# Performance work log

Measured on AMD Instinct MI355X. Metric: run time of the kernel, lower is better.

Reference implementation:

```python
import jax, jax.numpy as jnp
import numpy as np

B, S, D, H, F = 8, 1024, 1024, 16, 4096
DH = D // H  # 64
EPS = 1e-12


def _layer_norm(x, g, b):
    mu = jnp.mean(x, axis=-1, keepdims=True)
    var = jnp.mean(jnp.square(x - mu), axis=-1, keepdims=True)
    return (x - mu) / jnp.sqrt(var + EPS) * g + b


def setup_inputs() -> dict:
    key = jax.random.key(0)
    ks = jax.random.split(key, 16)
    sd = 0.02
    inp = {
        "x": jax.random.normal(ks[0], (B, S, D), dtype=jnp.float32),
        "attn_mask": jnp.ones((B, S), dtype=jnp.int32),
        # attention projections (torch Linear: W is [out, in])
        "Wq": jax.random.normal(ks[1], (D, D), dtype=jnp.float32) * sd,
        "bq": jnp.zeros((D,), dtype=jnp.float32),
        "Wk": jax.random.normal(ks[2], (D, D), dtype=jnp.float32) * sd,
        "bk": jnp.zeros((D,), dtype=jnp.float32),
        "Wv": jax.random.normal(ks[3], (D, D), dtype=jnp.float32) * sd,
        "bv": jnp.zeros((D,), dtype=jnp.float32),
        "Wo": jax.random.normal(ks[4], (D, D), dtype=jnp.float32) * sd,
        "bo": jnp.zeros((D,), dtype=jnp.float32),
        # sa_layer_norm
        "ln1_g": jnp.ones((D,), dtype=jnp.float32),
        "ln1_b": jnp.zeros((D,), dtype=jnp.float32),
        # FFN
        "W1": jax.random.normal(ks[5], (F, D), dtype=jnp.float32) * sd,
        "b1": jnp.zeros((F,), dtype=jnp.float32),
        "W2": jax.random.normal(ks[6], (D, F), dtype=jnp.float32) * sd,
        "b2": jnp.zeros((D,), dtype=jnp.float32),
        # output_layer_norm
        "ln2_g": jnp.ones((D,), dtype=jnp.float32),
        "ln2_b": jnp.zeros((D,), dtype=jnp.float32),
    }
    return inp


def reference(x, attn_mask, Wq, bq, Wk, bk, Wv, bv, Wo, bo,
              ln1_g, ln1_b, W1, b1, W2, b2, ln2_g, ln2_b):
    b, s, d = x.shape

    def proj_heads(inp, W, bias):
        y = jnp.einsum('bsd,ed->bse', inp, W) + bias  # torch Linear: x @ W.T + b
        return y.reshape(b, s, H, DH).transpose(0, 2, 1, 3)  # (b, h, s, dh)

    q = proj_heads(x, Wq, bq) / jnp.sqrt(jnp.float32(DH))
    k = proj_heads(x, Wk, bk)
    v = proj_heads(x, Wv, bv)

    scores = jnp.einsum('bhqe,bhke->bhqk', q, k)  # (b, h, s, s)
    pad = (attn_mask == 0)[:, None, None, :]      # (b, 1, 1, s)
    scores = jnp.where(pad, -jnp.inf, scores)
    weights = jax.nn.softmax(scores, axis=-1)

    ctx = jnp.einsum('bhqk,bhke->bhqe', weights, v)
    ctx = ctx.transpose(0, 2, 1, 3).reshape(b, s, d)
    sa_out = jnp.einsum('bsd,ed->bse', ctx, Wo) + bo

    h = _layer_norm(sa_out + x, ln1_g, ln1_b)

    ff = jnp.einsum('bsd,fd->bsf', h, W1) + b1
    ff = jax.nn.gelu(ff, approximate=False)
    ff = jnp.einsum('bsf,df->bsd', ff, W2) + b2

    out = _layer_norm(ff + h, ln2_g, ln2_b)
    return out
```

## Files before the change

### kernel.cpp

```cpp
#include <hip/hip_runtime.h>
#include <math.h>

typedef __attribute__((ext_vector_type(8))) short short8;
typedef __attribute__((ext_vector_type(4))) float f32x4;

__device__ __forceinline__ unsigned short f2bf(float f) {
  unsigned int u = __float_as_uint(f);
  u += 0x7fffu + ((u >> 16) & 1u);
  return (unsigned short)(u >> 16);
}

__device__ __forceinline__ float gelu_f(float v) {
  float xa = fabsf(v) * 0.70710678118f;
  float t = __builtin_amdgcn_rcpf(1.f + 0.3275911f * xa);
  float p = t * (0.254829592f +
            t * (-0.284496736f +
            t * (1.421413741f +
            t * (-1.453152027f + t * 1.061405429f))));
  float erfa = 1.f - p * __expf(-xa * xa);
  return 0.5f * v * (1.f + copysignf(erfa, v));
}

__device__ __forceinline__ void gll16(const unsigned short* g, unsigned short* l) {
  __builtin_amdgcn_global_load_lds(
      (const __attribute__((address_space(1))) unsigned int*)(uintptr_t)g,
      (__attribute__((address_space(3))) unsigned int*)(uintptr_t)l, 16, 0, 0);
}

__global__ __launch_bounds__(256) void cvt_all(
    const float* __restrict__ Wq, const float* __restrict__ Wk,
    const float* __restrict__ Wv, const float* __restrict__ Wo,
    const float* __restrict__ W1, const float* __restrict__ W2,
    const float* __restrict__ x, unsigned short* __restrict__ ws) {
  const int bi = blockIdx.x;
  const float* in;
  unsigned short* out;
  int i;
  if (bi < 4096) {
    const int m = bi >> 10;
    in = (m == 0) ? Wq : (m == 1) ? Wk : (m == 2) ? Wv : Wo;
    out = ws + (size_t)m * (1u << 20);
    i = (bi & 1023) * 256 + threadIdx.x;
  } else if (bi < 8192) {
    in = W1; out = ws + (4u << 20); i = (bi - 4096) * 256 + threadIdx.x;
  } else if (bi < 12288) {
    in = W2; out = ws + (8u << 20); i = (bi - 8192) * 256 + threadIdx.x;
  } else {
    in = x; out = ws + (12u << 20); i = (bi - 12288) * 256 + threadIdx.x;
  }
  float4 f = reinterpret_cast<const float4*>(in)[i];
  ushort4 o;
  o.x = f2bf(f.x); o.y = f2bf(f.y); o.z = f2bf(f.z); o.w = f2bf(f.w);
  reinterpret_cast<ushort4*>(out)[i] = o;
}

template <int EPI, bool SWAP>
__global__ __launch_bounds__(256) void gemm_nt(
    const unsigned short* __restrict__ A, const unsigned short* __restrict__ B,
    const float* __restrict__ bias, const float* __restrict__ bias_k,
    int K, int N, const float* __restrict__ resid,
    unsigned short* __restrict__ outb, float* __restrict__ outf) {
  __shared__ __align__(16) unsigned short As[2][128 * 32];
  __shared__ __align__(16) unsigned short Bs[2][128 * 32];
  const int t = threadIdx.x;
  const int tm = blockIdx.y * 128, tn = blockIdx.x * 128;
  const int lane = t & 63, wv = t >> 6;
  const int wr = wv >> 1, wc = wv & 1;
  const int l15 = lane & 15, quad = lane >> 4;
  const int srow = lane >> 2;
  const int scol = (lane & 3) << 3;

  const unsigned short* pa0 = &A[(size_t)(tm + wv * 32 + srow) * K + scol];
  const unsigned short* pa1 = &A[(size_t)(tm + wv * 32 + 16 + srow) * K + scol];
  const unsigned short* pb0 = &B[(size_t)(tn + wv * 32 + srow) * K + scol];
  const unsigned short* pb1 = &B[(size_t)(tn + wv * 32 + 16 + srow) * K + scol];
  unsigned short* la0 = &As[0][(wv * 2) * 512];
  unsigned short* la1 = &As[0][(wv * 2 + 1) * 512];
  unsigned short* lb0 = &Bs[0][(wv * 2) * 512];
  unsigned short* lb1 = &Bs[0][(wv * 2 + 1) * 512];

  const f32x4 zero = {0.f, 0.f, 0.f, 0.f};
  f32x4 acc[4][4];
#pragma unroll
  for (int i = 0; i < 4; ++i)
#pragma unroll
    for (int j = 0; j < 4; ++j) acc[i][j] = zero;

  gll16(pa0, la0); pa0 += 32;
  gll16(pa1, la1); pa1 += 32;
  gll16(pb0, lb0); pb0 += 32;
  gll16(pb1, lb1); pb1 += 32;

  const int nIter = K >> 5;
  for (int it = 0; it < nIter; ++it) {
    __syncthreads();
    const int cur = (it & 1) * 4096;
    const int nxt = 4096 - cur;
    if (it + 1 < nIter) {
      gll16(pa0, la0 + nxt); pa0 += 32;
      gll16(pa1, la1 + nxt); pa1 += 32;
      gll16(pb0, lb0 + nxt); pb0 += 32;
      gll16(pb1, lb1 + nxt); pb1 += 32;
    }
    short8 af[4], bfr[4];
#pragma unroll
    for (int i = 0; i < 4; ++i) {
      af[i] = *reinterpret_cast<const short8*>(&As[0][cur + (wr * 64 + i * 16 + l15) * 32 + quad * 8]);
      bfr[i] = *reinterpret_cast<const short8*>(&Bs[0][cur + (wc * 64 + i * 16 + l15) * 32 + quad * 8]);
    }
#pragma unroll
    for (int i = 0; i < 4; ++i)
#pragma unroll
      for (int j = 0; j < 4; ++j)
        acc[i][j] = SWAP
            ? __builtin_amdgcn_mfma_f32_16x16x32_bf16(bfr[j], af[i], acc[i][j], 0, 0, 0)
            : __builtin_amdgcn_mfma_f32_16x16x32_bf16(af[i], bfr[j], acc[i][j], 0, 0, 0);
  }

  if (SWAP) {
#pragma unroll
    for (int i = 0; i < 4; ++i) {
      const int row = tm + wr * 64 + i * 16 + l15;
#pragma unroll
      for (int j = 0; j < 4; ++j) {
        const int col0 = tn + wc * 64 + j * 16 + quad * 4;
        if (EPI == 5) {
          const int chunk = col0 >> 10;
          const int colc = col0 & 1023;
          const float4 b4 = *reinterpret_cast<const float4*>(
              &(chunk == 0 ? bias : bias_k)[colc]);
          const float sc = (chunk == 0) ? 0.125f : 1.f;
          const int h = colc >> 6, dh = colc & 63;
          const int b = row >> 10, s = row & 1023;
          ushort4 pk;
          pk.x = f2bf((acc[i][j][0] + b4.x) * sc);
          pk.y = f2bf((acc[i][j][1] + b4.y) * sc);
          pk.z = f2bf((acc[i][j][2] + b4.z) * sc);
          pk.w = f2bf((acc[i][j][3] + b4.w) * sc);
          *reinterpret_cast<ushort4*>(
              &outb[((size_t)chunk << 23) + (((size_t)((b << 4) + h)) << 16) + (s << 6) + dh]) = pk;
        } else if (EPI == 2) {
          const float4 b4 = *reinterpret_cast<const float4*>(&bias[col0]);
          ushort4 pk;
          pk.x = f2bf(gelu_f(acc[i][j][0] + b4.x));
          pk.y = f2bf(gelu_f(acc[i][j][1] + b4.y));
          pk.z = f2bf(gelu_f(acc[i][j][2] + b4.z));
          pk.w = f2bf(gelu_f(acc[i][j][3] + b4.w));
          *reinterpret_cast<ushort4*>(&outb[(size_t)row * (size_t)N + col0]) = pk;
        } else {
          const float4 b4 = *reinterpret_cast<const float4*>(&bias[col0]);
          const size_t idx = (size_t)row * (size_t)N + col0;
          const float4 r4 = *reinterpret_cast<const float4*>(&resid[idx]);
          float4 o4;
          o4.x = acc[i][j][0] + b4.x + r4.x;
          o4.y = acc[i][j][1] + b4.y + r4.y;
          o4.z = acc[i][j][2] + b4.z + r4.z;
          o4.w = acc[i][j][3] + b4.w + r4.w;
          *reinterpret_cast<float4*>(&outf[idx]) = o4;
        }
      }
    }
  } else {
#pragma unroll
    for (int i = 0; i < 4; ++i) {
#pragma unroll
      for (int j = 0; j < 4; ++j) {
        const int col = tn + wc * 64 + j * 16 + l15;
        const float bcol = bias[col];
        const int h = col >> 6, dh = col & 63;
        const int row0 = tm + wr * 64 + i * 16 + quad * 4;
        const int b = row0 >> 10, s0 = row0 & 1023;
        ushort4 pk;
        pk.x = f2bf(acc[i][j][0] + bcol);
        pk.y = f2bf(acc[i][j][1] + bcol);
        pk.z = f2bf(acc[i][j][2] + bcol);
        pk.w = f2bf(acc[i][j][3] + bcol);
        *reinterpret_cast<ushort4*>(
            &outb[(((size_t)((b << 4) + h)) << 16) + (dh << 10) + s0]) = pk;
      }
    }
  }
}

__global__ __launch_bounds__(256) void attn_kernel(
    const unsigned short* __restrict__ Q, const unsigned short* __restrict__ Kc,
    const unsigned short* __restrict__ Vg, const int* __restrict__ mask,
    unsigned short* __restrict__ ctx) {
  __shared__ __align__(16) unsigned short Ks[2][64 * 64];
  __shared__ __align__(16) unsigned short Vs[2][64 * 64];
  __shared__ __align__(16) unsigned short Ps[4][16 * 72];
  __shared__ float maskf[1024];
  const int t = threadIdx.x;
  const int bh = blockIdx.x;
  const int qt = blockIdx.y;
  const int b = bh >> 4, h = bh & 15;
  const int lane = t & 63, wv = t >> 6, l15 = lane & 15, quad = lane >> 4;
  const int lr = lane >> 3;
  const int cs = (lane & 7) ^ lr;
  const unsigned short* Qp = Q + ((size_t)bh << 16);
  const unsigned short* Kp = Kc + ((size_t)bh << 16);
  const unsigned short* Vp = Vg + ((size_t)bh << 16);
  const int seg0 = wv * 2, seg1 = wv * 2 + 1;
  const int r0 = seg0 * 8 + lr, r1 = seg1 * 8 + lr;

  for (int i = t; i < 1024; i += 256)
    maskf[i] = mask[b * 1024 + i] ? -8.f : -INFINITY;

  short8 qf[2][2];
#pragma unroll
  for (int g = 0; g < 2; ++g)
#pragma unroll
    for (int hh = 0; hh < 2; ++hh)
      qf[g][hh] = *reinterpret_cast<const short8*>(
          &Qp[(size_t)(qt * 128 + wv * 32 + g * 16 + l15) * 64 + hh * 32 + quad * 8]);

  gll16(&Kp[r0 * 64 + cs * 8], &Ks[0][seg0 * 512]);
  gll16(&Kp[r1 * 64 + cs * 8], &Ks[0][seg1 * 512]);
  gll16(&Vp[r0 * 1024 + cs * 8], &Vs[0][seg0 * 512]);
  gll16(&Vp[r1 * 1024 + cs * 8], &Vs[0][seg1 * 512]);

  const int sw0 = ((quad ^ (l15 & 7)) << 3);
  const int sw1 = (((quad + 4) ^ (l15 & 7)) << 3);
  const f32x4 zero = {0.f, 0.f, 0.f, 0.f};
  float ps[2][4];
  f32x4 o[2][4];
#pragma unroll
  for (int g = 0; g < 2; ++g)
#pragma unroll
    for (int j = 0; j < 4; ++j) { o[g][j] = zero; ps[g][j] = 0.f; }

  unsigned short* Pw = Ps[wv];
  for (int kt = 0; kt < 16; ++kt) {
    __syncthreads();
    const int cur = kt & 1;
    if (kt < 15) {
      const int nb = cur ^ 1;
      gll16(&Kp[((kt + 1) * 64 + r0) * 64 + cs * 8], &Ks[nb][seg0 * 512]);
      gll16(&Kp[((kt + 1) * 64 + r1) * 64 + cs * 8], &Ks[nb][seg1 * 512]);
      gll16(&Vp[r0 * 1024 + (kt + 1) * 64 + cs * 8], &Vs[nb][seg0 * 512]);
      gll16(&Vp[r1 * 1024 + (kt + 1) * 64 + cs * 8], &Vs[nb][seg1 * 512]);
    }
    float madd[4];
    short8 kf[4][2];
#pragma unroll
    for (int nt = 0; nt < 4; ++nt) {
      const int row = (nt * 16 + l15) * 64;
      kf[nt][0] = *reinterpret_cast<const short8*>(&Ks[cur][row + sw0]);
      kf[nt][1] = *reinterpret_cast<const short8*>(&Ks[cur][row + sw1]);
      madd[nt] = maskf[kt * 64 + nt * 16 + l15];
    }
#pragma unroll
    for (int g = 0; g < 2; ++g) {
      f32x4 s4[4];
#pragma unroll
      for (int nt = 0; nt < 4; ++nt) {
        s4[nt] = __builtin_amdgcn_mfma_f32_16x16x32_bf16(qf[g][0], kf[nt][0], zero, 0, 0, 0);
        s4[nt] = __builtin_amdgcn_mfma_f32_16x16x32_bf16(qf[g][1], kf[nt][1], s4[nt], 0, 0, 0);
      }
#pragma unroll
      for (int nt = 0; nt < 4; ++nt) {
#pragma unroll
        for (int r = 0; r < 4; ++r) {
          float p = __expf(s4[nt][r] + madd[nt]);
          ps[g][r] += p;
          Pw[(quad * 4 + r) * 72 + nt * 16 + l15] = f2bf(p);
        }
      }
      short8 pf0 = *reinterpret_cast<const short8*>(&Pw[l15 * 72 + quad * 8]);
      short8 pf1 = *reinterpret_cast<const short8*>(&Pw[l15 * 72 + 32 + quad * 8]);
#pragma unroll
      for (int nt = 0; nt < 4; ++nt) {
        const int row = (nt * 16 + l15) * 64;
        short8 vf0 = *reinterpret_cast<const short8*>(&Vs[cur][row + sw0]);
        short8 vf1 = *reinterpret_cast<const short8*>(&Vs[cur][row + sw1]);
        o[g][nt] = __builtin_amdgcn_mfma_f32_16x16x32_bf16(pf0, vf0, o[g][nt], 0, 0, 0);
        o[g][nt] = __builtin_amdgcn_mfma_f32_16x16x32_bf16(pf1, vf1, o[g][nt], 0, 0, 0);
      }
    }
  }

#pragma unroll
  for (int g = 0; g < 2; ++g)
#pragma unroll
    for (int r = 0; r < 4; ++r) {
      float v = ps[g][r];
#pragma unroll
      for (int off = 8; off >= 1; off >>= 1) v += __shfl_xor(v, off, 64);
      const float inv = 1.f / v;
      const int srow = qt * 128 + wv * 32 + g * 16 + quad * 4 + r;
#pragma unroll
      for (int nt = 0; nt < 4; ++nt) {
        const int dh = nt * 16 + l15;
        ctx[((size_t)b << 20) + ((size_t)srow << 10) + (h << 6) + dh] =
            f2bf(o[g][nt][r] * inv);
      }
    }
}

__global__ __launch_bounds__(256) void ln_kernel(float* __restrict__ y,
                                                 const float* __restrict__ g,
                                                 const float* __restrict__ be,
                                                 unsigned short* __restrict__ hb) {
  __shared__ float sm[8];
  const int t = threadIdx.x;
  const size_t row = blockIdx.x;
  float* yr = y + (row << 10);
  float v[4];
#pragma unroll
  for (int i = 0; i < 4; ++i) v[i] = yr[t + (i << 8)];
  float s = v[0] + v[1] + v[2] + v[3];
#pragma unroll
  for (int off = 32; off >= 1; off >>= 1) s += __shfl_xor(s, off, 64);
  if ((t & 63) == 0) sm[t >> 6] = s;
  __syncthreads();
  float mu = (sm[0] + sm[1] + sm[2] + sm[3]) * (1.f / 1024.f);
  float q = 0.f;
#pragma unroll
  for (int i = 0; i < 4; ++i) { float d = v[i] - mu; q += d * d; }
#pragma unroll
  for (int off = 32; off >= 1; off >>= 1) q += __shfl_xor(q, off, 64);
  if ((t & 63) == 0) sm[4 + (t >> 6)] = q;
  __syncthreads();
  float var = (sm[4] + sm[5] + sm[6] + sm[7]) * (1.f / 1024.f);
  float rs = rsqrtf(var + 1e-12f);
#pragma unroll
  for (int i = 0; i < 4; ++i) {
    int c = t + (i << 8);
    float o = (v[i] - mu) * rs * g[c] + be[c];
    yr[c] = o;
    if (hb) hb[(row << 10) + c] = f2bf(o);
  }
}

extern "C" void kernel_launch(void* const* d_in, const int* in_sizes, int n_in,
                              void* d_out, int out_size, void* d_ws, size_t ws_size,
                              hipStream_t stream) {
  const float* x   = (const float*)d_in[0];
  const int*   msk = (const int*)d_in[1];
  const float* Wq  = (const float*)d_in[2];
  const float* bq  = (const float*)d_in[3];
  const float* Wk  = (const float*)d_in[4];
  const float* bk  = (const float*)d_in[5];
  const float* Wv  = (const float*)d_in[6];
  const float* bv  = (const float*)d_in[7];
  const float* Wo  = (const float*)d_in[8];
  const float* bo  = (const float*)d_in[9];
  const float* g1  = (const float*)d_in[10];
  const float* be1 = (const float*)d_in[11];
  const float* W1  = (const float*)d_in[12];
  const float* b1  = (const float*)d_in[13];
  const float* W2  = (const float*)d_in[14];
  const float* b2  = (const float*)d_in[15];
  const float* g2  = (const float*)d_in[16];
  const float* be2 = (const float*)d_in[17];
  float* out = (float*)d_out;

  unsigned short* Wqb = (unsigned short*)d_ws;
  unsigned short* Wvb = Wqb + (2u << 20);
  unsigned short* Wob = Wvb + (1u << 20);
  unsigned short* W1b = Wob + (1u << 20);
  unsigned short* W2b = W1b + (4u << 20);
  unsigned short* xb  = W2b + (4u << 20);
  unsigned short* qb  = xb + (8u << 20);
  unsigned short* vb  = qb + (16u << 20);
  unsigned short* ctx = xb;
  unsigned short* ffb = xb;
  float* y1 = (float*)(qb + (24u << 20));
  unsigned short* hb = (unsigned short*)(y1 + (8u << 20));

  dim3 blk(256);
  cvt_all<<<dim3(20480), blk, 0, stream>>>(Wq, Wk, Wv, Wo, W1, W2, x, (unsigned short*)d_ws);
  gemm_nt<5, true><<<dim3(16, 64), blk, 0, stream>>>(xb, Wqb, bq, bk, 1024, 1024,
                                                     nullptr, qb, nullptr);
  gemm_nt<4, false><<<dim3(8, 64), blk, 0, stream>>>(xb, Wvb, bv, nullptr, 1024, 1024,
                                                     nullptr, vb, nullptr);
  attn_kernel<<<dim3(128, 8), blk, 0, stream>>>(qb, qb + (8u << 20), vb, msk, ctx);
  gemm_nt<1, true><<<dim3(8, 64), blk, 0, stream>>>(ctx, Wob, bo, nullptr, 1024, 1024,
                                                    x, nullptr, y1);
  ln_kernel<<<dim3(8192), blk, 0, stream>>>(y1, g1, be1, hb);
  gemm_nt<2, true><<<dim3(32, 64), blk, 0, stream>>>(hb, W1b, b1, nullptr, 1024, 4096,
                                                     nullptr, ffb, nullptr);
  gemm_nt<1, true><<<dim3(8, 64), blk, 0, stream>>>(ffb, W2b, b2, nullptr, 4096, 1024,
                                                    y1, nullptr, out);
  ln_kernel<<<dim3(8192), blk, 0, stream>>>(out, g2, be2, nullptr);
}
```

Before: 550.9 us.

## Add 256-row 512-thread GEMM with ping-pong LDS pipeline for big projections

Adds a new gemm_big kernel with 256xBN tiles, 8 waves, double-buffered LDS filled by direct global-to-LDS loads, staged waitcnt/barrier scheduling, MFMA priority boosting, and an XCD-aware block remap. The QK projection, output projection and both FFN GEMMs now use it in place of the 128x128 kernel. The goal is more reuse per LDS byte and better overlap of loads with MFMA work. In exchange the kernel has high register pressure from 8xNREP accumulators and produces fewer blocks, which may lower occupancy or leave a partial wave of tiles.

```diff
diff --git a/kernel.cpp b/kernel.cpp
--- a/kernel.cpp
+++ b/kernel.cpp
@@ -124,22 +124,7 @@
 #pragma unroll
       for (int j = 0; j < 4; ++j) {
         const int col0 = tn + wc * 64 + j * 16 + quad * 4;
-        if (EPI == 5) {
-          const int chunk = col0 >> 10;
-          const int colc = col0 & 1023;
-          const float4 b4 = *reinterpret_cast<const float4*>(
-              &(chunk == 0 ? bias : bias_k)[colc]);
-          const float sc = (chunk == 0) ? 0.125f : 1.f;
-          const int h = colc >> 6, dh = colc & 63;
-          const int b = row >> 10, s = row & 1023;
-          ushort4 pk;
-          pk.x = f2bf((acc[i][j][0] + b4.x) * sc);
-          pk.y = f2bf((acc[i][j][1] + b4.y) * sc);
-          pk.z = f2bf((acc[i][j][2] + b4.z) * sc);
-          pk.w = f2bf((acc[i][j][3] + b4.w) * sc);
-          *reinterpret_cast<ushort4*>(
-              &outb[((size_t)chunk << 23) + (((size_t)((b << 4) + h)) << 16) + (s << 6) + dh]) = pk;
-        } else if (EPI == 2) {
+        if (EPI == 2) {
           const float4 b4 = *reinterpret_cast<const float4*>(&bias[col0]);
           ushort4 pk;
           pk.x = f2bf(gelu_f(acc[i][j][0] + b4.x));
@@ -181,6 +166,211 @@
     }
   }
 }
+
+#define MFMA_Q(mh, nh)                                                        \
+  {                                                                           \
+    __builtin_amdgcn_s_setprio(1);                                            \
+    _Pragma("unroll") for (int i = 0; i < 4; ++i) {                           \
+      _Pragma("unroll") for (int jj = 0; jj < NREP / 2; ++jj) {               \
+        const int j = (nh) * (NREP / 2) + jj;                                 \
+        acc[(mh) * 4 + i][j] = __builtin_amdgcn_mfma_f32_16x16x32_bf16(       \
+            bf[j][0], af[i][0], acc[(mh) * 4 + i][j], 0, 0, 0);               \
+        acc[(mh) * 4 + i][j] = __builtin_amdgcn_mfma_f32_16x16x32_bf16(       \
+            bf[j][1], af[i][1], acc[(mh) * 4 + i][j], 0, 0, 0);               \
+      }                                                                       \
+    }                                                                         \
+    __builtin_amdgcn_s_setprio(0);                                            \
+  }
+
+#define READ_A(mh)                                                            \
+  _Pragma("unroll") for (int i = 0; i < 4; ++i) {                             \
+    af[i][0] = *reinterpret_cast<const short8*>(                              \
+        &Asc[abase + ((mh) * 64 + i * 16) * 64 + s0]);                        \
+    af[i][1] = *reinterpret_cast<const short8*>(                              \
+        &Asc[abase + ((mh) * 64 + i * 16) * 64 + s1]);                        \
+  }
+
+#define LGKM0                                                                 \
+  asm volatile("s_waitcnt lgkmcnt(0)" ::: "memory");                          \
+  __builtin_amdgcn_sched_barrier(0)
+
+#define MEMFENCE asm volatile("" ::: "memory")
+
+template <int EPI, int BN>
+__global__ __launch_bounds__(512, 2) void gemm_big(
+    const unsigned short* __restrict__ A, const unsigned short* __restrict__ B,
+    const float* __restrict__ bias, const float* __restrict__ bias_k,
+    int K, int N, const float* __restrict__ resid,
+    unsigned short* __restrict__ outb, float* __restrict__ outf) {
+  constexpr int WN = BN / 4;
+  constexpr int NREP = WN / 16;
+  constexpr int BGRP = BN / 64;
+  __shared__ __align__(16) unsigned short As[2][256 * 64];
+  __shared__ __align__(16) unsigned short Bs[2][BN * 64];
+
+  const int t = threadIdx.x;
+  const int lane = t & 63, wv = t >> 6;
+  const int wm = wv >> 2, wn = wv & 3;
+  const int l15 = lane & 15, quad = lane >> 4;
+
+  const int gx = gridDim.x;
+  const int nwg = gx * gridDim.y;
+  int lin = blockIdx.y * gx + blockIdx.x;
+  lin = (lin & 7) * (nwg >> 3) + (lin >> 3);
+  const int gxs = 31 - __clz(gx);
+  const int tn = (lin & (gx - 1)) * BN;
+  const int tm = (lin >> gxs) * 256;
+
+  const int srow = lane >> 3;
+  const int scol = ((lane & 7) ^ srow) << 3;
+  const unsigned short* pA[4];
+  const unsigned short* pB[BGRP];
+#pragma unroll
+  for (int g = 0; g < 4; ++g)
+    pA[g] = &A[(size_t)(tm + g * 64 + wv * 8 + srow) * K + scol];
+#pragma unroll
+  for (int g = 0; g < BGRP; ++g)
+    pB[g] = &B[(size_t)(tn + g * 64 + wv * 8 + srow) * K + scol];
+
+  const int abase = (wm * 128 + l15) * 64;
+  const int bbase = (wn * WN + l15) * 64;
+  const int s0 = ((quad ^ (l15 & 7)) << 3);
+  const int s1 = (((quad + 4) ^ (l15 & 7)) << 3);
+
+  const f32x4 zero = {0.f, 0.f, 0.f, 0.f};
+  f32x4 acc[8][NREP];
+#pragma unroll
+  for (int i = 0; i < 8; ++i)
+#pragma unroll
+    for (int j = 0; j < NREP; ++j) acc[i][j] = zero;
+  short8 af[4][2], bf[NREP][2];
+
+#pragma unroll
+  for (int g = 0; g < 4; ++g) gll16(pA[g], &As[0][(g * 64 + wv * 8) * 64]);
+#pragma unroll
+  for (int g = 0; g < BGRP; ++g) gll16(pB[g], &Bs[0][(g * 64 + wv * 8) * 64]);
+#pragma unroll
+  for (int g = 0; g < 4; ++g) {
+    pA[g] += 64;
+    gll16(pA[g], &As[1][(g * 64 + wv * 8) * 64]);
+    pA[g] += 64;
+  }
+#pragma unroll
+  for (int g = 0; g < BGRP; ++g) {
+    pB[g] += 64;
+    gll16(pB[g], &Bs[1][(g * 64 + wv * 8) * 64]);
+    pB[g] += 64;
+  }
+  if constexpr (BGRP == 4) asm volatile("s_waitcnt vmcnt(8)" ::: "memory");
+  else asm volatile("s_waitcnt vmcnt(6)" ::: "memory");
+  __builtin_amdgcn_s_barrier();
+  MEMFENCE;
+
+  const int NT = K >> 6;
+  for (int tt = 0; tt < NT; ++tt) {
+    const unsigned short* Asc = As[tt & 1];
+    const unsigned short* Bsc = Bs[tt & 1];
+    unsigned short* Asw = As[tt & 1];
+    unsigned short* Bsw = Bs[tt & 1];
+    const bool st = (tt + 2 < NT);
+
+    READ_A(0);
+#pragma unroll
+    for (int j = 0; j < NREP; ++j) {
+      bf[j][0] = *reinterpret_cast<const short8*>(&Bsc[bbase + (j * 16) * 64 + s0]);
+      bf[j][1] = *reinterpret_cast<const short8*>(&Bsc[bbase + (j * 16) * 64 + s1]);
+    }
+    LGKM0;
+    MFMA_Q(0, 0);
+    MFMA_Q(0, 1);
+    __builtin_amdgcn_s_barrier();
+    MEMFENCE;
+    if (st) {
+      gll16(pA[0], &Asw[(0 * 64 + wv * 8) * 64]);
+      gll16(pA[2], &Asw[(2 * 64 + wv * 8) * 64]);
+      gll16(pB[0], &Bsw[(0 * 64 + wv * 8) * 64]);
+      if constexpr (BGRP == 4) gll16(pB[1], &Bsw[(1 * 64 + wv * 8) * 64]);
+    }
+    READ_A(1);
+    LGKM0;
+    MFMA_Q(1, 0);
+    __builtin_amdgcn_s_barrier();
+    MEMFENCE;
+    if (st) {
+      gll16(pA[1], &Asw[(1 * 64 + wv * 8) * 64]);
+      gll16(pA[3], &Asw[(3 * 64 + wv * 8) * 64]);
+      if constexpr (BGRP == 4) {
+        gll16(pB[2], &Bsw[(2 * 64 + wv * 8) * 64]);
+        gll16(pB[3], &Bsw[(3 * 64 + wv * 8) * 64]);
+      } else {
+        gll16(pB[1], &Bsw[(1 * 64 + wv * 8) * 64]);
+      }
+#pragma unroll
+      for (int g = 0; g < 4; ++g) pA[g] += 64;
+#pragma unroll
+      for (int g = 0; g < BGRP; ++g) pB[g] += 64;
+    }
+    MFMA_Q(1, 1);
+    if (st) {
+      if constexpr (BGRP == 4) asm volatile("s_waitcnt vmcnt(8)" ::: "memory");
+      else asm volatile("s_waitcnt vmcnt(6)" ::: "memory");
+    } else {
+      asm volatile("s_waitcnt vmcnt(0)" ::: "memory");
+    }
+    __builtin_amdgcn_s_barrier();
+    MEMFENCE;
+  }
+
+  const int rb = tm + wm * 128 + l15;
+  const int cb = tn + wn * WN + (quad << 2);
+#pragma unroll
+  for (int i = 0; i < 8; ++i) {
+    const int row = rb + i * 16;
+#pragma unroll
+    for (int j = 0; j < NREP; ++j) {
+      const int col0 = cb + j * 16;
+      if constexpr (EPI == 5) {
+        const int chunk = col0 >> 10;
+        const int colc = col0 & 1023;
+        const float4 b4 = *reinterpret_cast<const float4*>(
+            &(chunk == 0 ? bias : bias_k)[colc]);
+        const float sc = (chunk == 0) ? 0.125f : 1.f;
+        const int h = colc >> 6, dh = colc & 63;
+        const int b = row >> 10, s = row & 1023;
+        ushort4 pk;
+        pk.x = f2bf((acc[i][j][0] + b4.x) * sc);
+        pk.y = f2bf((acc[i][j][1] + b4.y) * sc);
+        pk.z = f2bf((acc[i][j][2] + b4.z) * sc);
+        pk.w = f2bf((acc[i][j][3] + b4.w) * sc);
+        *reinterpret_cast<ushort4*>(
+            &outb[((size_t)chunk << 23) + (((size_t)((b << 4) + h)) << 16) +
+                  (s << 6) + dh]) = pk;
+      } else if constexpr (EPI == 2) {
+        const float4 b4 = *reinterpret_cast<const float4*>(&bias[col0]);
+        ushort4 pk;
+        pk.x = f2bf(gelu_f(acc[i][j][0] + b4.x));
+        pk.y = f2bf(gelu_f(acc[i][j][1] + b4.y));
+        pk.z = f2bf(gelu_f(acc[i][j][2] + b4.z));
+        pk.w = f2bf(gelu_f(acc[i][j][3] + b4.w));
+        *reinterpret_cast<ushort4*>(&outb[(size_t)row * (size_t)N + col0]) = pk;
+      } else {
+        const float4 b4 = *reinterpret_cast<const float4*>(&bias[col0]);
+        const size_t idx = (size_t)row * (size_t)N + col0;
+        const float4 r4 = *reinterpret_cast<const float4*>(&resid[idx]);
+        float4 o4;
+        o4.x = acc[i][j][0] + b4.x + r4.x;
+        o4.y = acc[i][j][1] + b4.y + r4.y;
+        o4.z = acc[i][j][2] + b4.z + r4.z;
+        o4.w = acc[i][j][3] + b4.w + r4.w;
+        *reinterpret_cast<float4*>(&outf[idx]) = o4;
+      }
+    }
+  }
+}
+#undef MFMA_Q
+#undef READ_A
+#undef LGKM0
+#undef MEMFENCE
 
 __global__ __launch_bounds__(256) void attn_kernel(
     const unsigned short* __restrict__ Q, const unsigned short* __restrict__ Kc,
@@ -368,19 +558,19 @@
   float* y1 = (float*)(qb + (24u << 20));
   unsigned short* hb = (unsigned short*)(y1 + (8u << 20));
 
-  dim3 blk(256);
+  dim3 blk(256), blk5(512);
   cvt_all<<<dim3(20480), blk, 0, stream>>>(Wq, Wk, Wv, Wo, W1, W2, x, (unsigned short*)d_ws);
-  gemm_nt<5, true><<<dim3(16, 64), blk, 0, stream>>>(xb, Wqb, bq, bk, 1024, 1024,
+  gemm_big<5, 256><<<dim3(8, 32), blk5, 0, stream>>>(xb, Wqb, bq, bk, 1024, 2048,
                                                      nullptr, qb, nullptr);
   gemm_nt<4, false><<<dim3(8, 64), blk, 0, stream>>>(xb, Wvb, bv, nullptr, 1024, 1024,
                                                      nullptr, vb, nullptr);
   attn_kernel<<<dim3(128, 8), blk, 0, stream>>>(qb, qb + (8u << 20), vb, msk, ctx);
-  gemm_nt<1, true><<<dim3(8, 64), blk, 0, stream>>>(ctx, Wob, bo, nullptr, 1024, 1024,
-                                                    x, nullptr, y1);
+  gemm_big<1, 128><<<dim3(8, 32), blk5, 0, stream>>>(ctx, Wob, bo, nullptr, 1024, 1024,
+                                                     x, nullptr, y1);
   ln_kernel<<<dim3(8192), blk, 0, stream>>>(y1, g1, be1, hb);
-  gemm_nt<2, true><<<dim3(32, 64), blk, 0, stream>>>(hb, W1b, b1, nullptr, 1024, 4096,
-                                                     nullptr, ffb, nullptr);
-  gemm_nt<1, true><<<dim3(8, 64), blk, 0, stream>>>(ffb, W2b, b2, nullptr, 4096, 1024,
-                                                    y1, nullptr, out);
+  gemm_big<2, 256><<<dim3(16, 32), blk5, 0, stream>>>(hb, W1b, b1, nullptr, 1024, 4096,
+                                                      nullptr, ffb, nullptr);
+  gemm_big<1, 128><<<dim3(8, 32), blk5, 0, stream>>>(ffb, W2b, b2, nullptr, 4096, 1024,
+                                                     y1, nullptr, out);
   ln_kernel<<<dim3(8192), blk, 0, stream>>>(out, g2, be2, nullptr);
 }
```

Measured after the change: 501.5 us. 1.1x faster.
